# Optimization experiments

Hardware: AMD Instinct MI355X
Metric: run time of the kernel (lower is better)

## Reference

```python
import jax, jax.numpy as jnp
import numpy as np

N, E, F_IN, H, C = 10000, 640000, 128, 128, 40


def setup_inputs() -> dict:
    key = jax.random.key(0)
    ks = jax.random.split(key, 8)
    x = jax.random.normal(ks[0], (N, F_IN), dtype=jnp.float32)
    edge_index = jax.random.randint(ks[1], (2, E), 0, N, dtype=jnp.int64)
    W1 = jax.random.normal(ks[2], (F_IN, H), dtype=jnp.float32) / np.sqrt(F_IN)
    b1 = jnp.zeros((H,), dtype=jnp.float32)
    W2 = jax.random.normal(ks[3], (H, H), dtype=jnp.float32) / np.sqrt(H)
    b2 = jnp.zeros((H,), dtype=jnp.float32)
    Wc = jax.random.normal(ks[4], (H, C), dtype=jnp.float32) / np.sqrt(H)
    bc = jnp.zeros((C,), dtype=jnp.float32)
    return {"x": x, "edge_index": edge_index, "W1": W1, "b1": b1,
            "W2": W2, "b2": b2, "Wc": Wc, "bc": bc}


def _gcn_conv(x, src, dst, norm, W, b):
    # GCNConv: out = D^{-1/2}(A+I)D^{-1/2} (x @ W) + b
    h = x @ W                               # [N, H]
    msg = h[src] * norm[:, None]            # gather + per-edge normalize
    out = jax.ops.segment_sum(msg, dst, num_segments=N)  # scatter-add
    return out + b


def reference(x, edge_index, W1, b1, W2, b2, Wc, bc):
    # add self-loops (as PyG GCNConv does by default)
    loops = jnp.arange(N, dtype=edge_index.dtype)
    src = jnp.concatenate([edge_index[0], loops])   # [E+N]
    dst = jnp.concatenate([edge_index[1], loops])   # [E+N]
    # symmetric normalization deg^{-1/2} with self-loops included
    deg = jax.ops.segment_sum(jnp.ones_like(dst, dtype=x.dtype), dst, num_segments=N)
    dinv = jax.lax.rsqrt(deg)                       # deg >= 1 due to self-loops
    norm = dinv[src] * dinv[dst]                    # [E+N]

    h = _gcn_conv(x, src, dst, norm, W1, b1)
    h = jax.nn.relu(h)
    h = _gcn_conv(h, src, dst, norm, W2, b2)
    logits = h @ Wc + bc                            # [N, C]
    return jax.nn.log_softmax(logits, axis=1)
```

## Files before the change

### kernel.cpp

```cpp
#include <hip/hip_runtime.h>
#include <hip/hip_fp16.h>
#include <math.h>

#define FDIM 128
#define CDIM 40
#define DMAX 192
#define NMAX 10240
#define SLICE_SHIFT 14
#define SLICE_SZ (1 << SLICE_SHIFT)

__device__ __forceinline__ uint2 pack_half4(float4 v) {
    __half2 p0 = __float22half2_rn(make_float2(v.x, v.y));
    __half2 p1 = __float22half2_rn(make_float2(v.z, v.w));
    uint2 u;
    u.x = *(unsigned int*)&p0;
    u.y = *(unsigned int*)&p1;
    return u;
}

__device__ __forceinline__ void upadd(float& a0, float& a1, unsigned int u) {
    __half2 h = *(__half2*)&u;
    float2 f = __half22float2(h);
    a0 += f.x; a1 += f.y;
}

__global__ __launch_bounds__(1024) void k_hist(
        const int* __restrict__ dst, unsigned short* __restrict__ lrank,
        int* __restrict__ cnt, int e, int n) {
    __shared__ int h[NMAX];
    int tid = threadIdx.x;
    for (int i = tid; i < n; i += 1024) h[i] = 0;
    __syncthreads();
    int base = (int)blockIdx.x << SLICE_SHIFT;
    int end = base + SLICE_SZ; if (end > e) end = e;
    for (int i = base + tid * 4; i < end; i += 4096) {
        if (i + 3 < end) {
            int4 d = *(const int4*)(dst + i);
            int p0 = atomicAdd(&h[d.x], 1);
            int p1 = atomicAdd(&h[d.y], 1);
            int p2 = atomicAdd(&h[d.z], 1);
            int p3 = atomicAdd(&h[d.w], 1);
            ushort4 r;
            r.x = (unsigned short)p0; r.y = (unsigned short)p1;
            r.z = (unsigned short)p2; r.w = (unsigned short)p3;
            *(ushort4*)(lrank + i) = r;
        } else {
            for (int k = i; k < end; ++k)
                lrank[k] = (unsigned short)atomicAdd(&h[dst[k]], 1);
        }
    }
    __syncthreads();
    int* c = cnt + (size_t)blockIdx.x * n;
    for (int i = tid; i < n; i += 1024) c[i] = h[i];
}

__global__ __launch_bounds__(256) void k_scan_wc(
        int* __restrict__ cnt, int* __restrict__ deg, int nslice, int n,
        int scanB, const float* __restrict__ W2, const float* __restrict__ Wc,
        const float* __restrict__ b2, const float* __restrict__ bc,
        float* __restrict__ W2c, float* __restrict__ bias2c) {
    int tid = threadIdx.x;
    if ((int)blockIdx.x < scanB) {
        int v = blockIdx.x * 256 + tid;
        if (v >= n) return;
        int s = 0;
        for (int b = 0; b < nslice; ++b) {
            int t = cnt[(size_t)b * n + v];
            cnt[(size_t)b * n + v] = s;
            s += t;
        }
        deg[v] = s;
    } else {
        int o = ((int)blockIdx.x - scanB) * 256 + tid;
        if (o >= FDIM * CDIM) return;
        int k = o / CDIM, c = o - k * CDIM;
        float acc = 0.f;
        for (int j = 0; j < FDIM; ++j)
            acc += W2[k * FDIM + j] * Wc[j * CDIM + c];
        W2c[o] = acc;
        if (o < CDIM) {
            float b = bc[o];
            for (int j = 0; j < FDIM; ++j)
                b += b2[j] * Wc[j * CDIM + o];
            bias2c[o] = b;
        }
    }
}

__global__ __launch_bounds__(256) void k_mega(
        const float* __restrict__ A, const float* __restrict__ W,
        const int* __restrict__ deg, uint2* __restrict__ h16, int n,
        const int* __restrict__ src, const int* __restrict__ dst,
        const unsigned short* __restrict__ lrank, const int* __restrict__ base,
        unsigned short* __restrict__ col, int e, int gemm_blocks) {
    __shared__ float As[32][FDIM];
    int tid = threadIdx.x;
    if ((int)blockIdx.x < gemm_blocks) {
        int r0 = blockIdx.x * 32;
        for (int t = tid; t < 32 * 32; t += 256) {
            int r = t >> 5, c4 = t & 31;
            int gr = r0 + r;
            float4 v = make_float4(0.f, 0.f, 0.f, 0.f);
            if (gr < n) v = ((const float4*)A)[(size_t)gr * 32 + c4];
            ((float4*)As[r])[c4] = v;
        }
        __syncthreads();
        int cb = (tid & 31) * 4;
        int rb = (tid >> 5) * 4;
        float4 acc0 = make_float4(0,0,0,0), acc1 = acc0, acc2 = acc0, acc3 = acc0;
        for (int k = 0; k < FDIM; ++k) {
            float4 w = *(const float4*)(W + k * FDIM + cb);
            float a0 = As[rb + 0][k], a1 = As[rb + 1][k];
            float a2 = As[rb + 2][k], a3 = As[rb + 3][k];
            acc0.x += a0 * w.x; acc0.y += a0 * w.y; acc0.z += a0 * w.z; acc0.w += a0 * w.w;
            acc1.x += a1 * w.x; acc1.y += a1 * w.y; acc1.z += a1 * w.z; acc1.w += a1 * w.w;
            acc2.x += a2 * w.x; acc2.y += a2 * w.y; acc2.z += a2 * w.z; acc2.w += a2 * w.w;
            acc3.x += a3 * w.x; acc3.y += a3 * w.y; acc3.z += a3 * w.z; acc3.w += a3 * w.w;
        }
        float4 accs[4] = {acc0, acc1, acc2, acc3};
        #pragma unroll
        for (int i = 0; i < 4; ++i) {
            int gr = r0 + rb + i;
            if (gr < n) {
                float dinv = rsqrtf((float)(deg[gr] + 1));
                float4 v = accs[i];
                v.x *= dinv; v.y *= dinv; v.z *= dinv; v.w *= dinv;
                h16[(size_t)gr * 32 + (cb >> 2)] = pack_half4(v);
            }
        }
    } else {
        int g = ((int)blockIdx.x - gemm_blocks) * 256 + tid;
        int i4 = g * 4;
        if (i4 + 3 < e) {
            const int* bs = base + (size_t)(i4 >> SLICE_SHIFT) * n;
            int4 d = ((const int4*)dst)[g];
            int4 s = ((const int4*)src)[g];
            ushort4 lr = ((const ushort4*)lrank)[g];
            int p0 = bs[d.x] + lr.x;
            int p1 = bs[d.y] + lr.y;
            int p2 = bs[d.z] + lr.z;
            int p3 = bs[d.w] + lr.w;
            if (p0 < DMAX) col[(size_t)d.x * DMAX + p0] = (unsigned short)s.x;
            if (p1 < DMAX) col[(size_t)d.y * DMAX + p1] = (unsigned short)s.y;
            if (p2 < DMAX) col[(size_t)d.z * DMAX + p2] = (unsigned short)s.z;
            if (p3 < DMAX) col[(size_t)d.w * DMAX + p3] = (unsigned short)s.w;
        } else if (i4 < e) {
            for (int k = i4; k < e; ++k) {
                int d = dst[k];
                int p = base[(size_t)(k >> SLICE_SHIFT) * n + d] + lrank[k];
                if (p < DMAX) col[(size_t)d * DMAX + p] = (unsigned short)src[k];
            }
        }
    }
}

__device__ __forceinline__ void wave_gather(
        float& o0, float& o1, const unsigned int* __restrict__ hs,
        const unsigned short* __restrict__ col, int node, int dn, int lane) {
    float a0 = 0.f, a1 = 0.f, b0 = 0.f, b1 = 0.f;
    upadd(a0, a1, hs[(size_t)node * 64 + lane]);
    const uint4* cl8 = (const uint4*)(col + (size_t)node * DMAX);
    int j = 0;
    for (; j + 16 <= dn; j += 16) {
        uint4 cA = cl8[(j >> 3)];
        uint4 cB = cl8[(j >> 3) + 1];
        int s0 = cA.x & 0xFFFF, s1 = cA.x >> 16;
        int s2 = cA.y & 0xFFFF, s3 = cA.y >> 16;
        int s4 = cA.z & 0xFFFF, s5 = cA.z >> 16;
        int s6 = cA.w & 0xFFFF, s7 = cA.w >> 16;
        int s8 = cB.x & 0xFFFF, s9 = cB.x >> 16;
        int sa = cB.y & 0xFFFF, sb = cB.y >> 16;
        int sc = cB.z & 0xFFFF, sd = cB.z >> 16;
        int se = cB.w & 0xFFFF, sf = cB.w >> 16;
        unsigned int q0 = hs[(size_t)s0 * 64 + lane];
        unsigned int q1 = hs[(size_t)s1 * 64 + lane];
        unsigned int q2 = hs[(size_t)s2 * 64 + lane];
        unsigned int q3 = hs[(size_t)s3 * 64 + lane];
        unsigned int q4 = hs[(size_t)s4 * 64 + lane];
        unsigned int q5 = hs[(size_t)s5 * 64 + lane];
        unsigned int q6 = hs[(size_t)s6 * 64 + lane];
        unsigned int q7 = hs[(size_t)s7 * 64 + lane];
        unsigned int q8 = hs[(size_t)s8 * 64 + lane];
        unsigned int q9 = hs[(size_t)s9 * 64 + lane];
        unsigned int qa = hs[(size_t)sa * 64 + lane];
        unsigned int qb = hs[(size_t)sb * 64 + lane];
        unsigned int qc = hs[(size_t)sc * 64 + lane];
        unsigned int qd = hs[(size_t)sd * 64 + lane];
        unsigned int qe = hs[(size_t)se * 64 + lane];
        unsigned int qf = hs[(size_t)sf * 64 + lane];
        upadd(a0, a1, q0); upadd(b0, b1, q1);
        upadd(a0, a1, q2); upadd(b0, b1, q3);
        upadd(a0, a1, q4); upadd(b0, b1, q5);
        upadd(a0, a1, q6); upadd(b0, b1, q7);
        upadd(a0, a1, q8); upadd(b0, b1, q9);
        upadd(a0, a1, qa); upadd(b0, b1, qb);
        upadd(a0, a1, qc); upadd(b0, b1, qd);
        upadd(a0, a1, qe); upadd(b0, b1, qf);
    }
    for (; j + 8 <= dn; j += 8) {
        uint4 c = cl8[j >> 3];
        int s0 = c.x & 0xFFFF, s1 = c.x >> 16;
        int s2 = c.y & 0xFFFF, s3 = c.y >> 16;
        int s4 = c.z & 0xFFFF, s5 = c.z >> 16;
        int s6 = c.w & 0xFFFF, s7 = c.w >> 16;
        unsigned int q0 = hs[(size_t)s0 * 64 + lane];
        unsigned int q1 = hs[(size_t)s1 * 64 + lane];
        unsigned int q2 = hs[(size_t)s2 * 64 + lane];
        unsigned int q3 = hs[(size_t)s3 * 64 + lane];
        unsigned int q4 = hs[(size_t)s4 * 64 + lane];
        unsigned int q5 = hs[(size_t)s5 * 64 + lane];
        unsigned int q6 = hs[(size_t)s6 * 64 + lane];
        unsigned int q7 = hs[(size_t)s7 * 64 + lane];
        upadd(a0, a1, q0); upadd(b0, b1, q1);
        upadd(a0, a1, q2); upadd(b0, b1, q3);
        upadd(a0, a1, q4); upadd(b0, b1, q5);
        upadd(a0, a1, q6); upadd(b0, b1, q7);
    }
    const unsigned short* cl = col + (size_t)node * DMAX;
    for (; j < dn; ++j) upadd(a0, a1, hs[(size_t)cl[j] * 64 + lane]);
    o0 = a0 + b0;
    o1 = a1 + b1;
}

__global__ __launch_bounds__(512) void k_agg1f(
        const unsigned int* __restrict__ hs1, const unsigned short* __restrict__ col,
        const int* __restrict__ deg, const float* __restrict__ b1,
        const float* __restrict__ W2c, float* __restrict__ z, int n) {
    __shared__ float Ws[FDIM * CDIM];
    __shared__ float As[8][FDIM];
    int tid = threadIdx.x;
    for (int t = tid; t < FDIM * CDIM; t += 512) Ws[t] = W2c[t];
    __syncthreads();
    int wv = tid >> 6, lane = tid & 63;
    int node = blockIdx.x * 8 + wv;
    if (node >= n) return;
    int dn = deg[node];
    float dinv = rsqrtf((float)(dn + 1));
    int dnc = dn > DMAX ? DMAX : dn;
    float o0, o1;
    wave_gather(o0, o1, hs1, col, node, dnc, lane);
    float2 bb = ((const float2*)b1)[lane];
    float v0 = fmaxf(dinv * o0 + bb.x, 0.f);
    float v1 = fmaxf(dinv * o1 + bb.y, 0.f);
    ((float2*)As[wv])[lane] = make_float2(v0, v1);
    int c = (lane < CDIM) ? lane : 0;
    const float* row = As[wv];
    float acc = 0.f;
    for (int k = 0; k < FDIM; k += 4) {
        float a0 = row[k + 0], a1 = row[k + 1];
        float a2 = row[k + 2], a3 = row[k + 3];
        acc += a0 * Ws[(k + 0) * CDIM + c];
        acc += a1 * Ws[(k + 1) * CDIM + c];
        acc += a2 * Ws[(k + 2) * CDIM + c];
        acc += a3 * Ws[(k + 3) * CDIM + c];
    }
    if (lane < CDIM) z[(size_t)node * CDIM + lane] = dinv * acc;
}

__global__ __launch_bounds__(512) void k_agg2s(
        const float* __restrict__ z, const unsigned short* __restrict__ col,
        const int* __restrict__ deg, const float* __restrict__ bias2c,
        float* __restrict__ out, int n) {
    int tid = threadIdx.x;
    int wv = tid >> 6, lane = tid & 63;
    int node = blockIdx.x * 8 + wv;
    if (node >= n) return;
    int dn = deg[node];
    float dinv = rsqrtf((float)(dn + 1));
    if (dn > DMAX) dn = DMAX;
    int cc = (lane < CDIM) ? lane : (lane - 24);
    const uint4* cl8 = (const uint4*)(col + (size_t)node * DMAX);
    float a = z[(size_t)node * CDIM + cc];
    float b = 0.f;
    int j = 0;
    for (; j + 16 <= dn; j += 16) {
        uint4 cA = cl8[(j >> 3)];
        uint4 cB = cl8[(j >> 3) + 1];
        int s0 = cA.x & 0xFFFF, s1 = cA.x >> 16;
        int s2 = cA.y & 0xFFFF, s3 = cA.y >> 16;
        int s4 = cA.z & 0xFFFF, s5 = cA.z >> 16;
        int s6 = cA.w & 0xFFFF, s7 = cA.w >> 16;
        int s8 = cB.x & 0xFFFF, s9 = cB.x >> 16;
        int sa = cB.y & 0xFFFF, sb = cB.y >> 16;
        int sc = cB.z & 0xFFFF, sd = cB.z >> 16;
        int se = cB.w & 0xFFFF, sf = cB.w >> 16;
        float q0 = z[(size_t)s0 * CDIM + cc];
        float q1 = z[(size_t)s1 * CDIM + cc];
        float q2 = z[(size_t)s2 * CDIM + cc];
        float q3 = z[(size_t)s3 * CDIM + cc];
        float q4 = z[(size_t)s4 * CDIM + cc];
        float q5 = z[(size_t)s5 * CDIM + cc];
        float q6 = z[(size_t)s6 * CDIM + cc];
        float q7 = z[(size_t)s7 * CDIM + cc];
        float q8 = z[(size_t)s8 * CDIM + cc];
        float q9 = z[(size_t)s9 * CDIM + cc];
        float qa = z[(size_t)sa * CDIM + cc];
        float qb = z[(size_t)sb * CDIM + cc];
        float qc = z[(size_t)sc * CDIM + cc];
        float qd = z[(size_t)sd * CDIM + cc];
        float qe = z[(size_t)se * CDIM + cc];
        float qf = z[(size_t)sf * CDIM + cc];
        a += q0; b += q1; a += q2; b += q3;
        a += q4; b += q5; a += q6; b += q7;
        a += q8; b += q9; a += qa; b += qb;
        a += qc; b += qd; a += qe; b += qf;
    }
    for (; j + 8 <= dn; j += 8) {
        uint4 c = cl8[j >> 3];
        int s0 = c.x & 0xFFFF, s1 = c.x >> 16;
        int s2 = c.y & 0xFFFF, s3 = c.y >> 16;
        int s4 = c.z & 0xFFFF, s5 = c.z >> 16;
        int s6 = c.w & 0xFFFF, s7 = c.w >> 16;
        float q0 = z[(size_t)s0 * CDIM + cc];
        float q1 = z[(size_t)s1 * CDIM + cc];
        float q2 = z[(size_t)s2 * CDIM + cc];
        float q3 = z[(size_t)s3 * CDIM + cc];
        float q4 = z[(size_t)s4 * CDIM + cc];
        float q5 = z[(size_t)s5 * CDIM + cc];
        float q6 = z[(size_t)s6 * CDIM + cc];
        float q7 = z[(size_t)s7 * CDIM + cc];
        a += q0; b += q1; a += q2; b += q3;
        a += q4; b += q5; a += q6; b += q7;
    }
    const unsigned short* cl = col + (size_t)node * DMAX;
    for (; j < dn; ++j) a += z[(size_t)cl[j] * CDIM + cc];
    float lv = (lane < CDIM) ? (dinv * (a + b) + bias2c[lane]) : -INFINITY;
    float m = lv;
    for (int off = 32; off > 0; off >>= 1) m = fmaxf(m, __shfl_down(m, off));
    m = __shfl(m, 0);
    float e = (lane < CDIM) ? expf(lv - m) : 0.0f;
    float s = e;
    for (int off = 32; off > 0; off >>= 1) s += __shfl_down(s, off);
    s = __shfl(s, 0);
    if (lane < CDIM) out[(size_t)node * CDIM + lane] = lv - m - logf(s);
}


extern "C" void kernel_launch(void* const* d_in, const int* in_sizes, int n_in,
                              void* d_out, int out_size, void* d_ws, size_t ws_size,
                              hipStream_t stream) {
    const float* x  = (const float*)d_in[0];
    const int*   ei = (const int*)d_in[1];
    const float* W1 = (const float*)d_in[2];
    const float* b1 = (const float*)d_in[3];
    const float* W2 = (const float*)d_in[4];
    const float* b2 = (const float*)d_in[5];
    const float* Wc = (const float*)d_in[6];
    const float* bc = (const float*)d_in[7];
    float* out = (float*)d_out;

    const int N = in_sizes[0] / FDIM;
    const int E = in_sizes[1] / 2;
    const int* srcp = ei;
    const int* dstp = ei + E;
    const int NSLICE = (E + SLICE_SZ - 1) >> SLICE_SHIFT;

    char* ws = (char*)d_ws;
    auto alloc = [&](size_t bytes) {
        char* p = ws;
        ws += (bytes + 255) & ~(size_t)255;
        return p;
    };
    int*            deg    = (int*)           alloc((size_t)N * 4);
    int*            cnt    = (int*)           alloc((size_t)NSLICE * N * 4);
    unsigned short* lrank  = (unsigned short*)alloc((size_t)E * 2);
    unsigned short* col    = (unsigned short*)alloc((size_t)N * DMAX * 2);
    uint4*          h1h    = (uint4*)         alloc((size_t)N * 256);
    float*          W2c    = (float*)         alloc((size_t)FDIM * CDIM * 4);
    float*          bias2c = (float*)         alloc((size_t)CDIM * 4);
    float*          z      = (float*)         alloc((size_t)N * CDIM * 4 + 256);

    k_hist<<<NSLICE, 1024, 0, stream>>>(dstp, lrank, cnt, E, N);

    int scanB = (N + 255) / 256;
    int wcB = (FDIM * CDIM + 255) / 256;
    k_scan_wc<<<scanB + wcB, 256, 0, stream>>>(
        cnt, deg, NSLICE, N, scanB, W2, Wc, b2, bc, W2c, bias2c);

    int gb = (N + 31) / 32;
    int fb = (E / 4 + 255) / 256;
    k_mega<<<gb + fb, 256, 0, stream>>>(
        x, W1, deg, (uint2*)h1h, N, srcp, dstp, lrank, cnt, col, E, gb);

    k_agg1f<<<(N + 7) / 8, 512, 0, stream>>>(
        (const unsigned int*)h1h, col, deg, b1, W2c, z, N);

    k_agg2s<<<(N + 7) / 8, 512, 0, stream>>>(z, col, deg, bias2c, out, N);
}
```

Measured before the change: 141.6 us.

## Overlap first GEMM with histogram, defer scaling, store layer-2 features as fp16

Moves the x@W1 GEMM into the histogram kernel as extra blocks, so it runs alongside the degree counting instead of in the later fill kernel. The GEMM writes unscaled fp32 to a new buffer, and a separate pass in the fill kernel applies deg^-1/2 and packs to half. The intermediate z for the second aggregation becomes fp16, halving its gather traffic. The cost is an extra fp32 write and read of h1, block size dropping from 1024 to 512 for the histogram, and lower precision in z.

```diff
diff --git a/kernel.cpp b/kernel.cpp
--- a/kernel.cpp
+++ b/kernel.cpp
@@ -24,34 +24,61 @@
     a0 += f.x; a1 += f.y;
 }
 
-__global__ __launch_bounds__(1024) void k_hist(
+__global__ __launch_bounds__(512) void k_hist_gemm(
         const int* __restrict__ dst, unsigned short* __restrict__ lrank,
-        int* __restrict__ cnt, int e, int n) {
+        int* __restrict__ cnt, int e, int n, int nslice,
+        const float* __restrict__ A, const float* __restrict__ W,
+        float* __restrict__ h1f) {
     __shared__ int h[NMAX];
     int tid = threadIdx.x;
-    for (int i = tid; i < n; i += 1024) h[i] = 0;
-    __syncthreads();
-    int base = (int)blockIdx.x << SLICE_SHIFT;
-    int end = base + SLICE_SZ; if (end > e) end = e;
-    for (int i = base + tid * 4; i < end; i += 4096) {
-        if (i + 3 < end) {
-            int4 d = *(const int4*)(dst + i);
-            int p0 = atomicAdd(&h[d.x], 1);
-            int p1 = atomicAdd(&h[d.y], 1);
-            int p2 = atomicAdd(&h[d.z], 1);
-            int p3 = atomicAdd(&h[d.w], 1);
-            ushort4 r;
-            r.x = (unsigned short)p0; r.y = (unsigned short)p1;
-            r.z = (unsigned short)p2; r.w = (unsigned short)p3;
-            *(ushort4*)(lrank + i) = r;
-        } else {
-            for (int k = i; k < end; ++k)
-                lrank[k] = (unsigned short)atomicAdd(&h[dst[k]], 1);
-        }
-    }
-    __syncthreads();
-    int* c = cnt + (size_t)blockIdx.x * n;
-    for (int i = tid; i < n; i += 1024) c[i] = h[i];
+    if ((int)blockIdx.x < nslice) {
+        for (int i = tid; i < n; i += 512) h[i] = 0;
+        __syncthreads();
+        int base = (int)blockIdx.x << SLICE_SHIFT;
+        int end = base + SLICE_SZ; if (end > e) end = e;
+        for (int i = base + tid * 4; i < end; i += 2048) {
+            if (i + 3 < end) {
+                int4 d = *(const int4*)(dst + i);
+                int p0 = atomicAdd(&h[d.x], 1);
+                int p1 = atomicAdd(&h[d.y], 1);
+                int p2 = atomicAdd(&h[d.z], 1);
+                int p3 = atomicAdd(&h[d.w], 1);
+                ushort4 r;
+                r.x = (unsigned short)p0; r.y = (unsigned short)p1;
+                r.z = (unsigned short)p2; r.w = (unsigned short)p3;
+                *(ushort4*)(lrank + i) = r;
+            } else {
+                for (int k = i; k < end; ++k)
+                    lrank[k] = (unsigned short)atomicAdd(&h[dst[k]], 1);
+            }
+        }
+        __syncthreads();
+        int* c = cnt + (size_t)blockIdx.x * n;
+        for (int i = tid; i < n; i += 512) c[i] = h[i];
+    } else {
+        float (*As)[FDIM] = (float (*)[FDIM])h;
+        int r0 = ((int)blockIdx.x - nslice) * 32;
+        for (int t = tid; t < 32 * 32; t += 512) {
+            int r = t >> 5, c4 = t & 31;
+            int gr = r0 + r;
+            float4 v = make_float4(0.f, 0.f, 0.f, 0.f);
+            if (gr < n) v = ((const float4*)A)[(size_t)gr * 32 + c4];
+            ((float4*)As[r])[c4] = v;
+        }
+        __syncthreads();
+        int cb = (tid & 31) * 4;
+        int rb = (tid >> 5) * 2;
+        float4 acc0 = make_float4(0,0,0,0), acc1 = acc0;
+        for (int k = 0; k < FDIM; ++k) {
+            float4 w = *(const float4*)(W + k * FDIM + cb);
+            float a0 = As[rb + 0][k], a1 = As[rb + 1][k];
+            acc0.x += a0 * w.x; acc0.y += a0 * w.y; acc0.z += a0 * w.z; acc0.w += a0 * w.w;
+            acc1.x += a1 * w.x; acc1.y += a1 * w.y; acc1.z += a1 * w.z; acc1.w += a1 * w.w;
+        }
+        int g0 = r0 + rb;
+        if (g0 < n)     ((float4*)h1f)[(size_t)g0 * 32 + (cb >> 2)] = acc0;
+        if (g0 + 1 < n) ((float4*)h1f)[(size_t)(g0 + 1) * 32 + (cb >> 2)] = acc1;
+    }
 }
 
 __global__ __launch_bounds__(256) void k_scan_wc(
@@ -87,49 +114,15 @@
     }
 }
 
-__global__ __launch_bounds__(256) void k_mega(
-        const float* __restrict__ A, const float* __restrict__ W,
-        const int* __restrict__ deg, uint2* __restrict__ h16, int n,
+__global__ __launch_bounds__(256) void k_fill_scale(
         const int* __restrict__ src, const int* __restrict__ dst,
         const unsigned short* __restrict__ lrank, const int* __restrict__ base,
-        unsigned short* __restrict__ col, int e, int gemm_blocks) {
-    __shared__ float As[32][FDIM];
-    int tid = threadIdx.x;
-    if ((int)blockIdx.x < gemm_blocks) {
-        int r0 = blockIdx.x * 32;
-        for (int t = tid; t < 32 * 32; t += 256) {
-            int r = t >> 5, c4 = t & 31;
-            int gr = r0 + r;
-            float4 v = make_float4(0.f, 0.f, 0.f, 0.f);
-            if (gr < n) v = ((const float4*)A)[(size_t)gr * 32 + c4];
-            ((float4*)As[r])[c4] = v;
-        }
-        __syncthreads();
-        int cb = (tid & 31) * 4;
-        int rb = (tid >> 5) * 4;
-        float4 acc0 = make_float4(0,0,0,0), acc1 = acc0, acc2 = acc0, acc3 = acc0;
-        for (int k = 0; k < FDIM; ++k) {
-            float4 w = *(const float4*)(W + k * FDIM + cb);
-            float a0 = As[rb + 0][k], a1 = As[rb + 1][k];
-            float a2 = As[rb + 2][k], a3 = As[rb + 3][k];
-            acc0.x += a0 * w.x; acc0.y += a0 * w.y; acc0.z += a0 * w.z; acc0.w += a0 * w.w;
-            acc1.x += a1 * w.x; acc1.y += a1 * w.y; acc1.z += a1 * w.z; acc1.w += a1 * w.w;
-            acc2.x += a2 * w.x; acc2.y += a2 * w.y; acc2.z += a2 * w.z; acc2.w += a2 * w.w;
-            acc3.x += a3 * w.x; acc3.y += a3 * w.y; acc3.z += a3 * w.z; acc3.w += a3 * w.w;
-        }
-        float4 accs[4] = {acc0, acc1, acc2, acc3};
-        #pragma unroll
-        for (int i = 0; i < 4; ++i) {
-            int gr = r0 + rb + i;
-            if (gr < n) {
-                float dinv = rsqrtf((float)(deg[gr] + 1));
-                float4 v = accs[i];
-                v.x *= dinv; v.y *= dinv; v.z *= dinv; v.w *= dinv;
-                h16[(size_t)gr * 32 + (cb >> 2)] = pack_half4(v);
-            }
-        }
-    } else {
-        int g = ((int)blockIdx.x - gemm_blocks) * 256 + tid;
+        unsigned short* __restrict__ col, int e, int fill_blocks,
+        const float* __restrict__ h1f, const int* __restrict__ deg,
+        uint2* __restrict__ h16, int n) {
+    int tid = threadIdx.x;
+    if ((int)blockIdx.x < fill_blocks) {
+        int g = (int)blockIdx.x * 256 + tid;
         int i4 = g * 4;
         if (i4 + 3 < e) {
             const int* bs = base + (size_t)(i4 >> SLICE_SHIFT) * n;
@@ -150,6 +143,17 @@
                 int p = base[(size_t)(k >> SLICE_SHIFT) * n + d] + lrank[k];
                 if (p < DMAX) col[(size_t)d * DMAX + p] = (unsigned short)src[k];
             }
+        }
+    } else {
+        int g = ((int)blockIdx.x - fill_blocks) * 256 + tid;
+        int t4 = n * 32;
+        int stride = ((int)gridDim.x - fill_blocks) * 256;
+        for (int idx = g; idx < t4; idx += stride) {
+            int node = idx >> 5;
+            float dinv = rsqrtf((float)(deg[node] + 1));
+            float4 v = ((const float4*)h1f)[idx];
+            v.x *= dinv; v.y *= dinv; v.z *= dinv; v.w *= dinv;
+            h16[idx] = pack_half4(v);
         }
     }
 }
@@ -225,7 +229,7 @@
 __global__ __launch_bounds__(512) void k_agg1f(
         const unsigned int* __restrict__ hs1, const unsigned short* __restrict__ col,
         const int* __restrict__ deg, const float* __restrict__ b1,
-        const float* __restrict__ W2c, float* __restrict__ z, int n) {
+        const float* __restrict__ W2c, __half* __restrict__ z, int n) {
     __shared__ float Ws[FDIM * CDIM];
     __shared__ float As[8][FDIM];
     int tid = threadIdx.x;
@@ -254,11 +258,11 @@
         acc += a2 * Ws[(k + 2) * CDIM + c];
         acc += a3 * Ws[(k + 3) * CDIM + c];
     }
-    if (lane < CDIM) z[(size_t)node * CDIM + lane] = dinv * acc;
+    if (lane < CDIM) z[(size_t)node * CDIM + lane] = __float2half(dinv * acc);
 }
 
 __global__ __launch_bounds__(512) void k_agg2s(
-        const float* __restrict__ z, const unsigned short* __restrict__ col,
+        const __half* __restrict__ z, const unsigned short* __restrict__ col,
         const int* __restrict__ deg, const float* __restrict__ bias2c,
         float* __restrict__ out, int n) {
     int tid = threadIdx.x;
@@ -270,7 +274,7 @@
     if (dn > DMAX) dn = DMAX;
     int cc = (lane < CDIM) ? lane : (lane - 24);
     const uint4* cl8 = (const uint4*)(col + (size_t)node * DMAX);
-    float a = z[(size_t)node * CDIM + cc];
+    float a = __half2float(z[(size_t)node * CDIM + cc]);
     float b = 0.f;
     int j = 0;
     for (; j + 16 <= dn; j += 16) {
@@ -284,22 +288,22 @@
         int sa = cB.y & 0xFFFF, sb = cB.y >> 16;
         int sc = cB.z & 0xFFFF, sd = cB.z >> 16;
         int se = cB.w & 0xFFFF, sf = cB.w >> 16;
-        float q0 = z[(size_t)s0 * CDIM + cc];
-        float q1 = z[(size_t)s1 * CDIM + cc];
-        float q2 = z[(size_t)s2 * CDIM + cc];
-        float q3 = z[(size_t)s3 * CDIM + cc];
-        float q4 = z[(size_t)s4 * CDIM + cc];
-        float q5 = z[(size_t)s5 * CDIM + cc];
-        float q6 = z[(size_t)s6 * CDIM + cc];
-        float q7 = z[(size_t)s7 * CDIM + cc];
-        float q8 = z[(size_t)s8 * CDIM + cc];
-        float q9 = z[(size_t)s9 * CDIM + cc];
-        float qa = z[(size_t)sa * CDIM + cc];
-        float qb = z[(size_t)sb * CDIM + cc];
-        float qc = z[(size_t)sc * CDIM + cc];
-        float qd = z[(size_t)sd * CDIM + cc];
-        float qe = z[(size_t)se * CDIM + cc];
-        float qf = z[(size_t)sf * CDIM + cc];
+        float q0 = __half2float(z[(size_t)s0 * CDIM + cc]);
+        float q1 = __half2float(z[(size_t)s1 * CDIM + cc]);
+        float q2 = __half2float(z[(size_t)s2 * CDIM + cc]);
+        float q3 = __half2float(z[(size_t)s3 * CDIM + cc]);
+        float q4 = __half2float(z[(size_t)s4 * CDIM + cc]);
+        float q5 = __half2float(z[(size_t)s5 * CDIM + cc]);
+        float q6 = __half2float(z[(size_t)s6 * CDIM + cc]);
+        float q7 = __half2float(z[(size_t)s7 * CDIM + cc]);
+        float q8 = __half2float(z[(size_t)s8 * CDIM + cc]);
+        float q9 = __half2float(z[(size_t)s9 * CDIM + cc]);
+        float qa = __half2float(z[(size_t)sa * CDIM + cc]);
+        float qb = __half2float(z[(size_t)sb * CDIM + cc]);
+        float qc = __half2float(z[(size_t)sc * CDIM + cc]);
+        float qd = __half2float(z[(size_t)sd * CDIM + cc]);
+        float qe = __half2float(z[(size_t)se * CDIM + cc]);
+        float qf = __half2float(z[(size_t)sf * CDIM + cc]);
         a += q0; b += q1; a += q2; b += q3;
         a += q4; b += q5; a += q6; b += q7;
         a += q8; b += q9; a += qa; b += qb;
@@ -311,19 +315,19 @@
         int s2 = c.y & 0xFFFF, s3 = c.y >> 16;
         int s4 = c.z & 0xFFFF, s5 = c.z >> 16;
         int s6 = c.w & 0xFFFF, s7 = c.w >> 16;
-        float q0 = z[(size_t)s0 * CDIM + cc];
-        float q1 = z[(size_t)s1 * CDIM + cc];
-        float q2 = z[(size_t)s2 * CDIM + cc];
-        float q3 = z[(size_t)s3 * CDIM + cc];
-        float q4 = z[(size_t)s4 * CDIM + cc];
-        float q5 = z[(size_t)s5 * CDIM + cc];
-        float q6 = z[(size_t)s6 * CDIM + cc];
-        float q7 = z[(size_t)s7 * CDIM + cc];
+        float q0 = __half2float(z[(size_t)s0 * CDIM + cc]);
+        float q1 = __half2float(z[(size_t)s1 * CDIM + cc]);
+        float q2 = __half2float(z[(size_t)s2 * CDIM + cc]);
+        float q3 = __half2float(z[(size_t)s3 * CDIM + cc]);
+        float q4 = __half2float(z[(size_t)s4 * CDIM + cc]);
+        float q5 = __half2float(z[(size_t)s5 * CDIM + cc]);
+        float q6 = __half2float(z[(size_t)s6 * CDIM + cc]);
+        float q7 = __half2float(z[(size_t)s7 * CDIM + cc]);
         a += q0; b += q1; a += q2; b += q3;
         a += q4; b += q5; a += q6; b += q7;
     }
     const unsigned short* cl = col + (size_t)node * DMAX;
-    for (; j < dn; ++j) a += z[(size_t)cl[j] * CDIM + cc];
+    for (; j < dn; ++j) a += __half2float(z[(size_t)cl[j] * CDIM + cc]);
     float lv = (lane < CDIM) ? (dinv * (a + b) + bias2c[lane]) : -INFINITY;
     float m = lv;
     for (int off = 32; off > 0; off >>= 1) m = fmaxf(m, __shfl_down(m, off));
@@ -365,22 +369,25 @@
     int*            cnt    = (int*)           alloc((size_t)NSLICE * N * 4);
     unsigned short* lrank  = (unsigned short*)alloc((size_t)E * 2);
     unsigned short* col    = (unsigned short*)alloc((size_t)N * DMAX * 2);
+    float*          h1f    = (float*)         alloc((size_t)N * FDIM * 4);
     uint4*          h1h    = (uint4*)         alloc((size_t)N * 256);
     float*          W2c    = (float*)         alloc((size_t)FDIM * CDIM * 4);
     float*          bias2c = (float*)         alloc((size_t)CDIM * 4);
-    float*          z      = (float*)         alloc((size_t)N * CDIM * 4 + 256);
-
-    k_hist<<<NSLICE, 1024, 0, stream>>>(dstp, lrank, cnt, E, N);
+    __half*         z      = (__half*)        alloc((size_t)N * CDIM * 2 + 256);
+
+    int gb = (N + 31) / 32;
+    k_hist_gemm<<<NSLICE + gb, 512, 0, stream>>>(
+        dstp, lrank, cnt, E, N, NSLICE, x, W1, h1f);
 
     int scanB = (N + 255) / 256;
     int wcB = (FDIM * CDIM + 255) / 256;
     k_scan_wc<<<scanB + wcB, 256, 0, stream>>>(
         cnt, deg, NSLICE, N, scanB, W2, Wc, b2, bc, W2c, bias2c);
 
-    int gb = (N + 31) / 32;
     int fb = (E / 4 + 255) / 256;
-    k_mega<<<gb + fb, 256, 0, stream>>>(
-        x, W1, deg, (uint2*)h1h, N, srcp, dstp, lrank, cnt, col, E, gb);
+    int sb = 160;
+    k_fill_scale<<<fb + sb, 256, 0, stream>>>(
+        srcp, dstp, lrank, cnt, col, E, fb, h1f, deg, (uint2*)h1h, N);
 
     k_agg1f<<<(N + 7) / 8, 512, 0, stream>>>(
         (const unsigned int*)h1h, col, deg, b1, W2c, z, N);
```

Result: slower. 145.9 us (+3.0%).
